# Optimization experiments

Measured on AMD Instinct MI355X. Metric: run time of the kernel, lower is better.

The kernel has to match this reference:

```python
import jax, jax.numpy as jnp
import numpy as np

N_NODES = 50000
N_EDGES = 400000
N_GRAPHS = 256
HID = 128
FEAT_IN, POS_IN, EDGE_IN = 64, 16, 16
N_LAYERS = 4


def _lin(x, w, b):
    return x @ w.T + b


def setup_inputs() -> dict:
    key = jax.random.key(0)
    ks = iter(jax.random.split(key, 64))
    s = 0.05

    def w(shape):
        return (jax.random.normal(next(ks), shape, dtype=jnp.float32) * s)

    inp = {
        "h": jax.random.normal(next(ks), (N_NODES, FEAT_IN), dtype=jnp.float32),
        "e": jax.random.normal(next(ks), (N_EDGES, EDGE_IN), dtype=jnp.float32),
        "p": jax.random.normal(next(ks), (N_NODES, POS_IN), dtype=jnp.float32),
        "edge_index": jax.random.randint(next(ks), (2, N_EDGES), 0, N_NODES),
        "batch": jnp.sort(jax.random.randint(next(ks), (N_NODES,), 0, N_GRAPHS)),
        # embeddings
        "h_embed_w": w((HID, FEAT_IN)), "h_embed_b": w((HID,)),
        "e_embed_w": w((HID, EDGE_IN)), "e_embed_b": w((HID,)),
        "p_embed_w": w((HID, POS_IN)), "p_embed_b": w((HID,)),
        # per-layer params, stacked over layers
        "hu_w": w((N_LAYERS, HID, 5 * HID)), "hu_b": w((N_LAYERS, HID)),
        "eu_w": w((N_LAYERS, HID, 3 * HID)), "eu_b": w((N_LAYERS, HID)),
        "pu_w": w((N_LAYERS, HID, 3 * HID)), "pu_b": w((N_LAYERS, HID)),
        "hagg_w": w((N_LAYERS, HID, 2 * HID)), "hagg_b": w((N_LAYERS, HID)),
        "pagg_w": w((N_LAYERS, HID, 2 * HID)), "pagg_b": w((N_LAYERS, HID)),
        # readout MLP
        "r1_w": w((HID, 2 * HID)), "r1_b": w((HID,)),
        "r2_w": w((HID // 2, HID)), "r2_b": w((HID // 2,)),
        "r3_w": w((1, HID // 2)), "r3_b": w((1,)),
    }
    return inp


def reference(h, e, p, edge_index, batch,
              h_embed_w, h_embed_b, e_embed_w, e_embed_b, p_embed_w, p_embed_b,
              hu_w, hu_b, eu_w, eu_b, pu_w, pu_b,
              hagg_w, hagg_b, pagg_w, pagg_b,
              r1_w, r1_b, r2_w, r2_b, r3_w, r3_b):
    send, rec = edge_index[0], edge_index[1]
    N = h.shape[0]

    h = _lin(h, h_embed_w, h_embed_b)
    e = _lin(e, e_embed_w, e_embed_b)
    p = _lin(p, p_embed_w, p_embed_b)

    for l in range(N_LAYERS):
        hp_send = jnp.concatenate((h[send], p[send]), axis=1)  # [E, 2H]
        hp_rec = jnp.concatenate((h[rec], p[rec]), axis=1)     # [E, 2H]
        h_msg = _lin(jnp.concatenate((hp_send, hp_rec, e), axis=1), hu_w[l], hu_b[l])
        h_msg_agg = jax.ops.segment_sum(h_msg, rec, num_segments=N)
        h = _lin(jnp.concatenate((h, h_msg_agg), axis=1), hagg_w[l], hagg_b[l])
        e = _lin(jnp.concatenate((h[send], h[rec], e), axis=1), eu_w[l], eu_b[l])
        p_msg = _lin(jnp.concatenate((p[send], p[rec], e), axis=1), pu_w[l], pu_b[l])
        p_msg_agg = jax.ops.segment_sum(p_msg, rec, num_segments=N)
        p = _lin(jnp.concatenate((p, p_msg_agg), axis=1), pagg_w[l], pagg_b[l])

    h_agg = jax.ops.segment_sum(h, batch, num_segments=N_GRAPHS)
    p_agg = jax.ops.segment_sum(p, batch, num_segments=N_GRAPHS)
    hep = jnp.concatenate((h_agg, p_agg), axis=1)
    x = jax.nn.relu(_lin(hep, r1_w, r1_b))
    x = jax.nn.relu(_lin(x, r2_w, r2_b))
    out = _lin(x, r3_w, r3_b).squeeze(-1)  # [N_GRAPHS]
    return (out, p)
```

## Files before the change

kernel.cpp:

```cpp
#include <hip/hip_runtime.h>

typedef __attribute__((ext_vector_type(8))) short bf16x8;
typedef __attribute__((ext_vector_type(4))) float f32x4;
typedef __attribute__((ext_vector_type(4))) unsigned short us4;
typedef __attribute__((ext_vector_type(2))) unsigned short us2;

__device__ __forceinline__ float b2f(unsigned short h) {
  union { unsigned int u; float f; } v; v.u = ((unsigned int)h) << 16; return v.f;
}
__device__ __forceinline__ unsigned short f2b(float f) {
  union { float f; unsigned int u; } v; v.f = f;
  unsigned int r = v.u + 0x7fffu + ((v.u >> 16) & 1u);
  return (unsigned short)(r >> 16);
}

__global__ void f2b_kernel(const float* __restrict__ in, unsigned short* __restrict__ out, int n4) {
  int i = blockIdx.x * blockDim.x + threadIdx.x;
  int stride = gridDim.x * blockDim.x;
  for (; i < n4; i += stride) {
    float4 v = reinterpret_cast<const float4*>(in)[i];
    us4 o;
    o[0] = f2b(v.x); o[1] = f2b(v.y); o[2] = f2b(v.z); o[3] = f2b(v.w);
    reinterpret_cast<us4*>(out)[i] = o;
  }
}

__launch_bounds__(256)
__global__ void compose_w(const float* __restrict__ hg, const float* __restrict__ hu,
                          const float* __restrict__ pg, const float* __restrict__ pu,
                          const float* __restrict__ hub, const float* __restrict__ pub,
                          unsigned short* __restrict__ wh, unsigned short* __restrict__ wp,
                          float* __restrict__ bh, float* __restrict__ bp) {
  __shared__ float As[128][129];
  __shared__ float Bs[128][132];
  __shared__ float bvs[128];
  const int l = blockIdx.x >> 3, t = blockIdx.x & 7;
  const float* A; const float* B; const float* bv; unsigned short* W; float* bo;
  int lda, ldb, K2, ldw, cbase;
  if (t < 5) {
    A = hg + (size_t)l * 128 * 256; lda = 256;
    B = hu + (size_t)l * 128 * 640; ldb = 640; K2 = 640;
    W = wh + (size_t)l * 128 * 768; ldw = 768;
    bv = hub + l * 128; bo = bh + l * 128; cbase = t * 128;
  } else {
    A = pg + (size_t)l * 128 * 256; lda = 256;
    B = pu + (size_t)l * 128 * 384; ldb = 384; K2 = 384;
    W = wp + (size_t)l * 128 * 512; ldw = 512;
    bv = pub + l * 128; bo = bp + l * 128; cbase = (t - 5) * 128;
  }
  const int tid = threadIdx.x;
  for (int idx = tid; idx < 128 * 128; idx += 256) {
    int r = idx >> 7, c = idx & 127;
    As[r][c] = A[r * lda + 128 + c];
    Bs[r][c] = B[r * ldb + cbase + c];
  }
  if (tid < 128) bvs[tid] = bv[tid];
  __syncthreads();
  const int o = tid & 127, g = tid >> 7;
  float acc[64];
#pragma unroll
  for (int j = 0; j < 64; ++j) acc[j] = 0.f;
  for (int m = 0; m < 128; ++m) {
    float a = As[o][m];
#pragma unroll
    for (int j4 = 0; j4 < 16; ++j4) {
      float4 b4 = *reinterpret_cast<const float4*>(&Bs[m][g * 64 + j4 * 4]);
      acc[j4 * 4 + 0] += a * b4.x; acc[j4 * 4 + 1] += a * b4.y;
      acc[j4 * 4 + 2] += a * b4.z; acc[j4 * 4 + 3] += a * b4.w;
    }
  }
#pragma unroll
  for (int j4 = 0; j4 < 16; ++j4) {
    us4 ov;
    ov[0] = f2b(acc[j4 * 4 + 0]); ov[1] = f2b(acc[j4 * 4 + 1]);
    ov[2] = f2b(acc[j4 * 4 + 2]); ov[3] = f2b(acc[j4 * 4 + 3]);
    *reinterpret_cast<us4*>(&W[(long)o * ldw + cbase + g * 64 + j4 * 4]) = ov;
  }
  if (cbase == 0) {
    for (int idx = tid; idx < 128 * 128; idx += 256) {
      int oo = idx >> 7, m = idx & 127;
      W[(long)oo * ldw + K2 + m] = f2b(A[oo * lda + m]);
    }
    if (tid < 128) {
      float s = 0.f;
      for (int m = 0; m < 128; ++m) s += As[tid][m] * bvs[m];
      bo[tid] = s;
    }
  }
}

template<int K>
__launch_bounds__(256)
__global__ void embed_fast(const float* __restrict__ in, const float* __restrict__ w,
                           const float* __restrict__ b, unsigned short* __restrict__ out,
                           long M, int ostride, int ocoloff, const float* __restrict__ degB,
                           unsigned short* __restrict__ out2, const float* __restrict__ scaleF) {
  __shared__ float wT[K][129];
  __shared__ float xt[16 * K];
  const int tid = threadIdx.x;
  const int col = tid & 127;
  const int half = tid >> 7;
  for (int idx = tid; idx < 128 * K; idx += 256) {
    int c = idx / K, k = idx % K;
    wT[k][c] = w[idx];
  }
  __syncthreads();
  float wreg[K];
#pragma unroll
  for (int k = 0; k < K; ++k) wreg[k] = wT[k][col];
  const float bcol = b[col];

  for (long r0 = (long)blockIdx.x * 16; r0 < M; r0 += (long)gridDim.x * 16) {
    __syncthreads();
    const float4* src4 = reinterpret_cast<const float4*>(in + r0 * K);
    const int n4 = 16 * K / 4;
    if (r0 + 16 <= M) {
      for (int i = tid; i < n4; i += 256)
        reinterpret_cast<float4*>(xt)[i] = src4[i];
    } else {
      int rem = (int)((M - r0) * K) / 4;
      for (int i = tid; i < n4; i += 256) {
        float4 z = {0.f, 0.f, 0.f, 0.f};
        reinterpret_cast<float4*>(xt)[i] = (i < rem) ? src4[i] : z;
      }
    }
    __syncthreads();
#pragma unroll
    for (int rr = 0; rr < 8; ++rr) {
      long row = r0 + half * 8 + rr;
      if (row >= M) break;
      const float* xr = &xt[(half * 8 + rr) * K];
      float acc = bcol * (degB ? degB[row] : 1.0f);
#pragma unroll
      for (int k4 = 0; k4 < K / 4; ++k4) {
        float4 xv = reinterpret_cast<const float4*>(xr)[k4];
        acc += xv.x * wreg[k4 * 4] + xv.y * wreg[k4 * 4 + 1] +
               xv.z * wreg[k4 * 4 + 2] + xv.w * wreg[k4 * 4 + 3];
      }
      long o = row * ostride + ocoloff + col;
      out[o] = f2b(acc);
      if (out2) out2[o] = f2b(acc * scaleF[row]);
    }
  }
}

__global__ void count_deg(const int* __restrict__ rec, int* __restrict__ deg, int E) {
  int i = blockIdx.x * blockDim.x + threadIdx.x;
  if (i < E) atomicAdd(&deg[rec[i]], 1);
}

__global__ void scan_blk(const int* __restrict__ deg, int* __restrict__ tmp,
                         int* __restrict__ blkSum, int N) {
  __shared__ int ts[256];
  const int b = blockIdx.x, t = threadIdx.x;
  const int base = b * 1024 + t * 4;
  int v0 = (base + 0 < N) ? deg[base + 0] : 0;
  int v1 = (base + 1 < N) ? deg[base + 1] : 0;
  int v2 = (base + 2 < N) ? deg[base + 2] : 0;
  int v3 = (base + 3 < N) ? deg[base + 3] : 0;
  int tsum = v0 + v1 + v2 + v3;
  ts[t] = tsum;
  __syncthreads();
  for (int off = 1; off < 256; off <<= 1) {
    int x = (t >= off) ? ts[t - off] : 0;
    __syncthreads();
    ts[t] += x;
    __syncthreads();
  }
  int texcl = ts[t] - tsum;
  if (base + 0 < N) tmp[base + 0] = texcl;
  if (base + 1 < N) tmp[base + 1] = texcl + v0;
  if (base + 2 < N) tmp[base + 2] = texcl + v0 + v1;
  if (base + 3 < N) tmp[base + 3] = texcl + v0 + v1 + v2;
  if (t == 255) blkSum[b] = ts[255];
}

__global__ void scan_top(int* __restrict__ blkSum, int nb) {
  __shared__ int s[64];
  int t = threadIdx.x;
  if (t < nb) s[t] = blkSum[t];
  __syncthreads();
  if (t == 0) {
    int run = 0;
    for (int i = 0; i < nb; ++i) { int x = s[i]; s[i] = run; run += x; }
  }
  __syncthreads();
  if (t < nb) blkSum[t] = s[t];
}

__global__ void scan_fix(const int* __restrict__ deg, int* __restrict__ row_ptr,
                         const int* __restrict__ blkOff, int* __restrict__ cursor,
                         float* __restrict__ degF, int N, int E) {
  const int b = blockIdx.x, t = threadIdx.x;
  const int base = b * 1024 + t * 4;
  const int off = blkOff[b];
#pragma unroll
  for (int k = 0; k < 4; ++k) {
    int i = base + k;
    if (i < N) {
      int v = row_ptr[i] + off;
      row_ptr[i] = v;
      cursor[i] = v;
      degF[i] = (float)deg[i];
    }
  }
  if (b == 0 && t == 0) row_ptr[N] = E;
}

__global__ void scatter_perm(const int* __restrict__ rec, const int* __restrict__ send,
                             int* __restrict__ cursor, int* __restrict__ perm,
                             int* __restrict__ sendP, int E) {
  int i = blockIdx.x * blockDim.x + threadIdx.x;
  if (i < E) {
    int pos = atomicAdd(&cursor[rec[i]], 1);
    perm[pos] = i;
    sendP[pos] = send[i];
  }
}

__global__ void segsum_raw(const float* __restrict__ eraw, const int* __restrict__ row_ptr,
                           const int* __restrict__ perm, float* __restrict__ out16, int N) {
  int sub = threadIdx.x >> 4;
  int f = threadIdx.x & 15;
  int r = blockIdx.x * 16 + sub;
  if (r >= N) return;
  int j0 = row_ptr[r], j1 = row_ptr[r + 1];
  float s0 = 0.f, s1 = 0.f;
  int j = j0;
  for (; j + 2 <= j1; j += 2) {
    int e0 = perm[j], e1 = perm[j + 1];
    s0 += eraw[(long)e0 * 16 + f];
    s1 += eraw[(long)e1 * 16 + f];
  }
  if (j < j1) s0 += eraw[(long)perm[j] * 16 + f];
  out16[(long)r * 16 + f] = s0 + s1;
}

__launch_bounds__(256)
__global__ void gather_sum256(const unsigned short* __restrict__ src,
                              const int* __restrict__ row_ptr, const int* __restrict__ sendP,
                              unsigned short* __restrict__ dst, int N) {
  const int wid = threadIdx.x >> 6, lane = threadIdx.x & 63;
  const int r = blockIdx.x * 4 + wid;
  if (r >= N) return;
  const int j0 = row_ptr[r], j1 = row_ptr[r + 1];
  const int off = lane * 4;
  float a0 = 0.f, a1 = 0.f, a2 = 0.f, a3 = 0.f;
  int j = j0;
  for (; j + 2 <= j1; j += 2) {
    int i0 = sendP[j], i1 = sendP[j + 1];
    us4 x = *reinterpret_cast<const us4*>(&src[(long)i0 * 256 + off]);
    us4 y = *reinterpret_cast<const us4*>(&src[(long)i1 * 256 + off]);
    a0 += b2f(x[0]) + b2f(y[0]); a1 += b2f(x[1]) + b2f(y[1]);
    a2 += b2f(x[2]) + b2f(y[2]); a3 += b2f(x[3]) + b2f(y[3]);
  }
  if (j < j1) {
    us4 x = *reinterpret_cast<const us4*>(&src[(long)sendP[j] * 256 + off]);
    a0 += b2f(x[0]); a1 += b2f(x[1]); a2 += b2f(x[2]); a3 += b2f(x[3]);
  }
  us4 o;
  o[0] = f2b(a0); o[1] = f2b(a1); o[2] = f2b(a2); o[3] = f2b(a3);
  *reinterpret_cast<us4*>(&dst[(long)r * 256 + off]) = o;
}

__launch_bounds__(256)
__global__ void gather_sum128(const unsigned short* __restrict__ src, int col,
                              const int* __restrict__ row_ptr, const int* __restrict__ sendP,
                              unsigned short* __restrict__ dst, int N) {
  const int wid = threadIdx.x >> 6, lane = threadIdx.x & 63;
  const int r = blockIdx.x * 4 + wid;
  if (r >= N) return;
  const int j0 = row_ptr[r], j1 = row_ptr[r + 1];
  const int half = lane >> 5;
  const int c = lane & 31;
  const int off = col + c * 4;
  float a0 = 0.f, a1 = 0.f, a2 = 0.f, a3 = 0.f;
  float b0 = 0.f, b1 = 0.f, b2 = 0.f, b3 = 0.f;
  int j = j0 + half;
  for (; j + 2 < j1; j += 4) {
    int i0 = sendP[j], i1 = sendP[j + 2];
    us4 x = *reinterpret_cast<const us4*>(&src[(long)i0 * 256 + off]);
    us4 y = *reinterpret_cast<const us4*>(&src[(long)i1 * 256 + off]);
    a0 += b2f(x[0]); a1 += b2f(x[1]); a2 += b2f(x[2]); a3 += b2f(x[3]);
    b0 += b2f(y[0]); b1 += b2f(y[1]); b2 += b2f(y[2]); b3 += b2f(y[3]);
  }
  if (j < j1) {
    us4 x = *reinterpret_cast<const us4*>(&src[(long)sendP[j] * 256 + off]);
    a0 += b2f(x[0]); a1 += b2f(x[1]); a2 += b2f(x[2]); a3 += b2f(x[3]);
  }
  a0 += b0; a1 += b1; a2 += b2; a3 += b3;
  a0 += __shfl_xor(a0, 32); a1 += __shfl_xor(a1, 32);
  a2 += __shfl_xor(a2, 32); a3 += __shfl_xor(a3, 32);
  if (half == 0) {
    us4 o;
    o[0] = f2b(a0); o[1] = f2b(a1); o[2] = f2b(a2); o[3] = f2b(a3);
    *reinterpret_cast<us4*>(&dst[(long)r * 256 + off]) = o;
  }
}

__launch_bounds__(256, 3)
__global__ void gemm_mp(int M, int nsrc, int strides, int coloffs,
                        const unsigned short* __restrict__ sp0, const unsigned short* __restrict__ sp1,
                        const unsigned short* __restrict__ sp2, const unsigned short* __restrict__ sp3,
                        const unsigned short* __restrict__ sp4, const unsigned short* __restrict__ sp5,
                        const unsigned short* __restrict__ Wb,
                        const float* __restrict__ bdeg, const float* __restrict__ bone,
                        const float* __restrict__ degF,
                        unsigned short* __restrict__ outB, int ostride, int ocoloff,
                        unsigned short* __restrict__ outB2, float* __restrict__ outF) {
  __shared__ __align__(16) unsigned short ldsW[8 * 64 * 8];
  const int tid = threadIdx.x;
  const int wid = tid >> 6, lane = tid & 63;
  const int K = nsrc * 128;
  const long rowBase = (long)blockIdx.x * 128 + wid * 32;
  const int lq = lane >> 4;
  const int lr = lane & 15;

  int rowD[2];
#pragma unroll
  for (int am = 0; am < 2; ++am) {
    long e = rowBase + am * 16 + lr;
    if (e >= M) e = M - 1;
    rowD[am] = (int)e;
  }

  f32x4 acc[2][8];
#pragma unroll
  for (int i = 0; i < 2; ++i)
#pragma unroll
    for (int j = 0; j < 8; ++j) acc[i][j] = 0.f;

  for (int si = 0; si < nsrc; ++si) {
    const unsigned short* sp = (si == 0) ? sp0 : (si == 1) ? sp1 : (si == 2) ? sp2
                              : (si == 3) ? sp3 : (si == 4) ? sp4 : sp5;
    const long astride = (long)(((strides >> (si * 4)) & 15) * 128);
    const int acoloff = ((coloffs >> (si * 4)) & 15) * 128;
#pragma unroll
    for (int sub = 0; sub < 4; ++sub) {
      const int koff = acoloff + sub * 32 + lq * 8;
      bf16x8 a[2];
#pragma unroll
      for (int am = 0; am < 2; ++am)
        a[am] = *reinterpret_cast<const bf16x8*>(&sp[(long)rowD[am] * astride + koff]);
      __syncthreads();
#pragma unroll
      for (int it = 0; it < 2; ++it) {
        int idx = tid + it * 256;
        int t = idx >> 6, l = idx & 63;
        int n = t * 16 + (l & 15);
        int kk = si * 128 + sub * 32 + ((l >> 4) * 8);
        *reinterpret_cast<bf16x8*>(&ldsW[idx * 8]) =
            *reinterpret_cast<const bf16x8*>(&Wb[(long)n * K + kk]);
      }
      __syncthreads();
#pragma unroll
      for (int n = 0; n < 8; ++n) {
        bf16x8 b = *reinterpret_cast<const bf16x8*>(&ldsW[(n * 64 + lane) * 8]);
#pragma unroll
        for (int am = 0; am < 2; ++am)
          acc[am][n] = __builtin_amdgcn_mfma_f32_16x16x32_bf16(a[am], b, acc[am][n], 0, 0, 0);
      }
    }
  }

  float bd[8], bo[8];
#pragma unroll
  for (int n = 0; n < 8; ++n) {
    bd[n] = bdeg ? bdeg[n * 16 + lr] : 0.f;
    bo[n] = bone ? bone[n * 16 + lr] : 0.f;
  }

#pragma unroll
  for (int am = 0; am < 2; ++am) {
#pragma unroll
    for (int r = 0; r < 4; ++r) {
      long row = rowBase + am * 16 + lq * 4 + r;
      if (row < M) {
        float d = degF[row];
        long ob = row * ostride + ocoloff;
#pragma unroll
        for (int n = 0; n < 8; ++n) {
          float v = acc[am][n][r] + bd[n] * d + bo[n];
          outB[ob + n * 16 + lr] = f2b(v);
          if (outB2) outB2[ob + n * 16 + lr] = f2b(v * d);
          if (outF) outF[row * 128 + n * 16 + lr] = v;
        }
      }
    }
  }
}

__global__ void readout_agg(const unsigned short* __restrict__ hp,
                            const int* __restrict__ batch, float* __restrict__ hep, int N) {
  int col = threadIdx.x;
  int n0 = blockIdx.x * 128;
  int n1 = n0 + 128; if (n1 > N) n1 = N;
  float sum = 0.f; int curg = -1;
  for (int n = n0; n < n1; ++n) {
    int g = batch[n];
    if (g != curg) {
      if (curg >= 0) unsafeAtomicAdd(&hep[(long)curg * 256 + col], sum);
      curg = g; sum = 0.f;
    }
    sum += b2f(hp[(long)n * 256 + col]);
  }
  if (curg >= 0) unsafeAtomicAdd(&hep[(long)curg * 256 + col], sum);
}

__global__ void mlp_kernel(const float* __restrict__ hep,
                           const float* __restrict__ r1w, const float* __restrict__ r1b,
                           const float* __restrict__ r2w, const float* __restrict__ r2b,
                           const float* __restrict__ r3w, const float* __restrict__ r3b,
                           float* __restrict__ out) {
  int g = blockIdx.x, t = threadIdx.x;
  __shared__ float x[256];
  __shared__ float y[128];
  __shared__ float z[64];
  x[t] = hep[(long)g * 256 + t];
  x[t + 128] = hep[(long)g * 256 + 128 + t];
  __syncthreads();
  float s = r1b[t];
  for (int k = 0; k < 256; ++k) s += r1w[t * 256 + k] * x[k];
  y[t] = fmaxf(s, 0.f);
  __syncthreads();
  if (t < 64) {
    float s2 = r2b[t];
    for (int k = 0; k < 128; ++k) s2 += r2w[t * 128 + k] * y[k];
    z[t] = fmaxf(s2, 0.f);
  }
  __syncthreads();
  if (t == 0) {
    float s3 = r3b[0];
    for (int k = 0; k < 64; ++k) s3 += r3w[k] * z[k];
    out[g] = s3;
  }
}

extern "C" void kernel_launch(void* const* d_in, const int* in_sizes, int n_in,
                              void* d_out, int out_size, void* d_ws, size_t ws_size,
                              hipStream_t stream) {
  const float* h_in = (const float*)d_in[0];
  const float* e_in = (const float*)d_in[1];
  const float* p_in = (const float*)d_in[2];
  const int* ei = (const int*)d_in[3];
  const int* batch = (const int*)d_in[4];
  const float* he_w = (const float*)d_in[5];  const float* he_b = (const float*)d_in[6];
  const float* ee_w = (const float*)d_in[7];  const float* ee_b = (const float*)d_in[8];
  const float* pe_w = (const float*)d_in[9];  const float* pe_b = (const float*)d_in[10];
  const float* hu_w = (const float*)d_in[11]; const float* hu_b = (const float*)d_in[12];
  const float* eu_w = (const float*)d_in[13]; const float* eu_b = (const float*)d_in[14];
  const float* pu_w = (const float*)d_in[15]; const float* pu_b = (const float*)d_in[16];
  const float* hg_w = (const float*)d_in[17]; const float* hg_b = (const float*)d_in[18];
  const float* pg_w = (const float*)d_in[19]; const float* pg_b = (const float*)d_in[20];
  const float* r1w = (const float*)d_in[21];  const float* r1b = (const float*)d_in[22];
  const float* r2w = (const float*)d_in[23];  const float* r2b = (const float*)d_in[24];
  const float* r3w = (const float*)d_in[25];  const float* r3b = (const float*)d_in[26];

  const int N = 50000, E = 400000, G = 256;
  const int* send = ei;
  const int* rec = ei + E;

  char* ws = (char*)d_ws;
  size_t off = 0;
  auto alloc = [&](size_t bytes) {
    void* pp = ws + off;
    off += (bytes + 255) & ~(size_t)255;
    return pp;
  };
  unsigned short* hp  = (unsigned short*)alloc((size_t)N * 256 * 2);
  unsigned short* dhp = (unsigned short*)alloc((size_t)N * 256 * 2);
  unsigned short* gHP = (unsigned short*)alloc((size_t)N * 256 * 2);
  unsigned short* sT  = (unsigned short*)alloc((size_t)N * 128 * 2);
  float* segsumF = (float*)alloc((size_t)N * 16 * 4);
  int* deg = (int*)alloc((size_t)N * 4);
  int* row_ptr = (int*)alloc((size_t)(N + 1) * 4);
  int* cursor = (int*)alloc((size_t)N * 4);
  int* blkSum = (int*)alloc((size_t)64 * 4);
  int* perm = (int*)alloc((size_t)E * 4);
  int* sendP = (int*)alloc((size_t)E * 4);
  float* degF = (float*)alloc((size_t)N * 4);
  float* hep = (float*)alloc((size_t)G * 256 * 4);
  unsigned short* w_h2 = (unsigned short*)alloc((size_t)4 * 128 * 768 * 2);
  unsigned short* w_p2 = (unsigned short*)alloc((size_t)4 * 128 * 512 * 2);
  unsigned short* w_eu = (unsigned short*)alloc((size_t)4 * 128 * 384 * 2);
  float* bh1 = (float*)alloc((size_t)4 * 128 * 4);
  float* bp1 = (float*)alloc((size_t)4 * 128 * 4);
  (void)ws_size; (void)n_in; (void)in_sizes; (void)out_size;

  f2b_kernel<<<192, 256, 0, stream>>>(eu_w, w_eu, 4 * 128 * 384 / 4);
  compose_w<<<32, 256, 0, stream>>>(hg_w, hu_w, pg_w, pu_w, hu_b, pu_b, w_h2, w_p2, bh1, bp1);

  const int nb = (N + 1023) / 1024;
  hipMemsetAsync(deg, 0, (size_t)N * 4, stream);
  count_deg<<<(E + 255) / 256, 256, 0, stream>>>(rec, deg, E);
  scan_blk<<<nb, 256, 0, stream>>>(deg, row_ptr, blkSum, N);
  scan_top<<<1, 64, 0, stream>>>(blkSum, nb);
  scan_fix<<<nb, 256, 0, stream>>>(deg, row_ptr, blkSum, cursor, degF, N, E);
  scatter_perm<<<(E + 255) / 256, 256, 0, stream>>>(rec, send, cursor, perm, sendP, E);

  embed_fast<64><<<3125, 256, 0, stream>>>(h_in, he_w, he_b, hp, N, 256, 0, nullptr, dhp, degF);
  embed_fast<16><<<3125, 256, 0, stream>>>(p_in, pe_w, pe_b, hp, N, 256, 128, nullptr, dhp, degF);
  segsum_raw<<<(N + 15) / 16, 256, 0, stream>>>(e_in, row_ptr, perm, segsumF, N);
  embed_fast<16><<<3125, 256, 0, stream>>>(segsumF, ee_w, ee_b, sT, N, 128, 0, degF, nullptr, nullptr);

  gather_sum256<<<(N + 3) / 4, 256, 0, stream>>>(hp, row_ptr, sendP, gHP, N);

  float* pOut = (float*)d_out + 256;
  const int gridN = (N + 127) / 128;
  const int gridG = (N + 3) / 4;

  for (int l = 0; l < 4; ++l) {
    gemm_mp<<<gridN, 256, 0, stream>>>(N, 6, 0x212222, 0x001010,
        gHP, gHP, dhp, dhp, sT, hp,
        w_h2 + (size_t)l * 128 * 768, bh1 + l * 128, hg_b + l * 128, degF,
        hp, 256, 0, dhp, nullptr);
    gather_sum128<<<gridG, 256, 0, stream>>>(hp, 0, row_ptr, sendP, gHP, N);
    gemm_mp<<<gridN, 256, 0, stream>>>(N, 3, 0x122, 0x000,
        gHP, dhp, sT, nullptr, nullptr, nullptr,
        w_eu + (size_t)l * 128 * 384, eu_b + l * 128, nullptr, degF,
        sT, 128, 0, nullptr, nullptr);
    gemm_mp<<<gridN, 256, 0, stream>>>(N, 4, 0x2122, 0x1011,
        gHP, dhp, sT, hp, nullptr, nullptr,
        w_p2 + (size_t)l * 128 * 512, bp1 + l * 128, pg_b + l * 128, degF,
        hp, 256, 128, (l < 3) ? dhp : nullptr, (l == 3) ? pOut : nullptr);
    if (l < 3)
      gather_sum128<<<gridG, 256, 0, stream>>>(hp, 128, row_ptr, sendP, gHP, N);
  }

  hipMemsetAsync(hep, 0, (size_t)G * 256 * 4, stream);
  readout_agg<<<(N + 127) / 128, 256, 0, stream>>>(hp, batch, hep, N);
  mlp_kernel<<<G, 128, 0, stream>>>(hep, r1w, r1b, r2w, r2b, r3w, r3b, (float*)d_out);
}
```

Measured before the change: 724.6 us.

## Drop degree-scaled copy buffer; apply degree scaling via separate MFMA accumulator

Removes the dhp buffer, which held degree-scaled copies of node features and was written by the embed and GEMM epilogues. Sources that need scaling now go into a second accumulator set (accS), and the epilogue multiplies that by degree before adding it. This cuts one bf16 store stream per GEMM and per embed, at the cost of double the accumulator registers, which may reduce occupancy under launch_bounds(256,3). It also splits compose_w into 128 smaller blocks for more parallelism, and scaling in fp32 rather than bf16 slightly changes rounding.

```diff
diff --git a/kernel.cpp b/kernel.cpp
--- a/kernel.cpp
+++ b/kernel.cpp
@@ -3,7 +3,6 @@
 typedef __attribute__((ext_vector_type(8))) short bf16x8;
 typedef __attribute__((ext_vector_type(4))) float f32x4;
 typedef __attribute__((ext_vector_type(4))) unsigned short us4;
-typedef __attribute__((ext_vector_type(2))) unsigned short us2;
 
 __device__ __forceinline__ float b2f(unsigned short h) {
   union { unsigned int u; float f; } v; v.u = ((unsigned int)h) << 16; return v.f;
@@ -32,49 +31,52 @@
                           unsigned short* __restrict__ wh, unsigned short* __restrict__ wp,
                           float* __restrict__ bh, float* __restrict__ bp) {
   __shared__ float As[128][129];
-  __shared__ float Bs[128][132];
+  __shared__ float Bs[128][36];
   __shared__ float bvs[128];
-  const int l = blockIdx.x >> 3, t = blockIdx.x & 7;
+  const int l = blockIdx.x >> 5, t = blockIdx.x & 31;
   const float* A; const float* B; const float* bv; unsigned short* W; float* bo;
   int lda, ldb, K2, ldw, cbase;
-  if (t < 5) {
+  if (t < 20) {
     A = hg + (size_t)l * 128 * 256; lda = 256;
     B = hu + (size_t)l * 128 * 640; ldb = 640; K2 = 640;
     W = wh + (size_t)l * 128 * 768; ldw = 768;
-    bv = hub + l * 128; bo = bh + l * 128; cbase = t * 128;
+    bv = hub + l * 128; bo = bh + l * 128; cbase = t * 32;
   } else {
     A = pg + (size_t)l * 128 * 256; lda = 256;
     B = pu + (size_t)l * 128 * 384; ldb = 384; K2 = 384;
     W = wp + (size_t)l * 128 * 512; ldw = 512;
-    bv = pub + l * 128; bo = bp + l * 128; cbase = (t - 5) * 128;
+    bv = pub + l * 128; bo = bp + l * 128; cbase = (t - 20) * 32;
   }
   const int tid = threadIdx.x;
   for (int idx = tid; idx < 128 * 128; idx += 256) {
     int r = idx >> 7, c = idx & 127;
     As[r][c] = A[r * lda + 128 + c];
-    Bs[r][c] = B[r * ldb + cbase + c];
+  }
+  for (int idx = tid; idx < 128 * 32; idx += 256) {
+    int m = idx >> 5, c = idx & 31;
+    Bs[m][c] = B[m * ldb + cbase + c];
   }
   if (tid < 128) bvs[tid] = bv[tid];
   __syncthreads();
   const int o = tid & 127, g = tid >> 7;
-  float acc[64];
-#pragma unroll
-  for (int j = 0; j < 64; ++j) acc[j] = 0.f;
+  float acc[16];
+#pragma unroll
+  for (int j = 0; j < 16; ++j) acc[j] = 0.f;
   for (int m = 0; m < 128; ++m) {
     float a = As[o][m];
 #pragma unroll
-    for (int j4 = 0; j4 < 16; ++j4) {
-      float4 b4 = *reinterpret_cast<const float4*>(&Bs[m][g * 64 + j4 * 4]);
+    for (int j4 = 0; j4 < 4; ++j4) {
+      float4 b4 = *reinterpret_cast<const float4*>(&Bs[m][g * 16 + j4 * 4]);
       acc[j4 * 4 + 0] += a * b4.x; acc[j4 * 4 + 1] += a * b4.y;
       acc[j4 * 4 + 2] += a * b4.z; acc[j4 * 4 + 3] += a * b4.w;
     }
   }
 #pragma unroll
-  for (int j4 = 0; j4 < 16; ++j4) {
+  for (int j4 = 0; j4 < 4; ++j4) {
     us4 ov;
     ov[0] = f2b(acc[j4 * 4 + 0]); ov[1] = f2b(acc[j4 * 4 + 1]);
     ov[2] = f2b(acc[j4 * 4 + 2]); ov[3] = f2b(acc[j4 * 4 + 3]);
-    *reinterpret_cast<us4*>(&W[(long)o * ldw + cbase + g * 64 + j4 * 4]) = ov;
+    *reinterpret_cast<us4*>(&W[(long)o * ldw + cbase + g * 16 + j4 * 4]) = ov;
   }
   if (cbase == 0) {
     for (int idx = tid; idx < 128 * 128; idx += 256) {
@@ -93,8 +95,7 @@
 __launch_bounds__(256)
 __global__ void embed_fast(const float* __restrict__ in, const float* __restrict__ w,
                            const float* __restrict__ b, unsigned short* __restrict__ out,
-                           long M, int ostride, int ocoloff, const float* __restrict__ degB,
-                           unsigned short* __restrict__ out2, const float* __restrict__ scaleF) {
+                           long M, int ostride, int ocoloff, const float* __restrict__ degB) {
   __shared__ float wT[K][129];
   __shared__ float xt[16 * K];
   const int tid = threadIdx.x;
@@ -137,9 +138,7 @@
         acc += xv.x * wreg[k4 * 4] + xv.y * wreg[k4 * 4 + 1] +
                xv.z * wreg[k4 * 4 + 2] + xv.w * wreg[k4 * 4 + 3];
       }
-      long o = row * ostride + ocoloff + col;
-      out[o] = f2b(acc);
-      if (out2) out2[o] = f2b(acc * scaleF[row]);
+      out[row * ostride + ocoloff + col] = f2b(acc);
     }
   }
 }
@@ -299,7 +298,7 @@
 }
 
 __launch_bounds__(256, 3)
-__global__ void gemm_mp(int M, int nsrc, int strides, int coloffs,
+__global__ void gemm_mp(int M, int nsrc, int strides, int coloffs, int smask,
                         const unsigned short* __restrict__ sp0, const unsigned short* __restrict__ sp1,
                         const unsigned short* __restrict__ sp2, const unsigned short* __restrict__ sp3,
                         const unsigned short* __restrict__ sp4, const unsigned short* __restrict__ sp5,
@@ -307,7 +306,7 @@
                         const float* __restrict__ bdeg, const float* __restrict__ bone,
                         const float* __restrict__ degF,
                         unsigned short* __restrict__ outB, int ostride, int ocoloff,
-                        unsigned short* __restrict__ outB2, float* __restrict__ outF) {
+                        float* __restrict__ outF) {
   __shared__ __align__(16) unsigned short ldsW[8 * 64 * 8];
   const int tid = threadIdx.x;
   const int wid = tid >> 6, lane = tid & 63;
@@ -324,17 +323,18 @@
     rowD[am] = (int)e;
   }
 
-  f32x4 acc[2][8];
+  f32x4 acc[2][8], accS[2][8];
 #pragma unroll
   for (int i = 0; i < 2; ++i)
 #pragma unroll
-    for (int j = 0; j < 8; ++j) acc[i][j] = 0.f;
+    for (int j = 0; j < 8; ++j) { acc[i][j] = 0.f; accS[i][j] = 0.f; }
 
   for (int si = 0; si < nsrc; ++si) {
     const unsigned short* sp = (si == 0) ? sp0 : (si == 1) ? sp1 : (si == 2) ? sp2
                               : (si == 3) ? sp3 : (si == 4) ? sp4 : sp5;
     const long astride = (long)(((strides >> (si * 4)) & 15) * 128);
     const int acoloff = ((coloffs >> (si * 4)) & 15) * 128;
+    const bool sc = (smask >> si) & 1;
 #pragma unroll
     for (int sub = 0; sub < 4; ++sub) {
       const int koff = acoloff + sub * 32 + lq * 8;
@@ -353,12 +353,22 @@
             *reinterpret_cast<const bf16x8*>(&Wb[(long)n * K + kk]);
       }
       __syncthreads();
-#pragma unroll
-      for (int n = 0; n < 8; ++n) {
-        bf16x8 b = *reinterpret_cast<const bf16x8*>(&ldsW[(n * 64 + lane) * 8]);
-#pragma unroll
-        for (int am = 0; am < 2; ++am)
-          acc[am][n] = __builtin_amdgcn_mfma_f32_16x16x32_bf16(a[am], b, acc[am][n], 0, 0, 0);
+      if (sc) {
+#pragma unroll
+        for (int n = 0; n < 8; ++n) {
+          bf16x8 b = *reinterpret_cast<const bf16x8*>(&ldsW[(n * 64 + lane) * 8]);
+#pragma unroll
+          for (int am = 0; am < 2; ++am)
+            accS[am][n] = __builtin_amdgcn_mfma_f32_16x16x32_bf16(a[am], b, accS[am][n], 0, 0, 0);
+        }
+      } else {
+#pragma unroll
+        for (int n = 0; n < 8; ++n) {
+          bf16x8 b = *reinterpret_cast<const bf16x8*>(&ldsW[(n * 64 + lane) * 8]);
+#pragma unroll
+          for (int am = 0; am < 2; ++am)
+            acc[am][n] = __builtin_amdgcn_mfma_f32_16x16x32_bf16(a[am], b, acc[am][n], 0, 0, 0);
+        }
       }
     }
   }
@@ -380,9 +390,8 @@
         long ob = row * ostride + ocoloff;
 #pragma unroll
         for (int n = 0; n < 8; ++n) {
-          float v = acc[am][n][r] + bd[n] * d + bo[n];
+          float v = acc[am][n][r] + d * accS[am][n][r] + bd[n] * d + bo[n];
           outB[ob + n * 16 + lr] = f2b(v);
-          if (outB2) outB2[ob + n * 16 + lr] = f2b(v * d);
           if (outF) outF[row * 128 + n * 16 + lr] = v;
         }
       }
@@ -468,7 +477,6 @@
     return pp;
   };
   unsigned short* hp  = (unsigned short*)alloc((size_t)N * 256 * 2);
-  unsigned short* dhp = (unsigned short*)alloc((size_t)N * 256 * 2);
   unsigned short* gHP = (unsigned short*)alloc((size_t)N * 256 * 2);
   unsigned short* sT  = (unsigned short*)alloc((size_t)N * 128 * 2);
   float* segsumF = (float*)alloc((size_t)N * 16 * 4);
@@ -488,7 +496,7 @@
   (void)ws_size; (void)n_in; (void)in_sizes; (void)out_size;
 
   f2b_kernel<<<192, 256, 0, stream>>>(eu_w, w_eu, 4 * 128 * 384 / 4);
-  compose_w<<<32, 256, 0, stream>>>(hg_w, hu_w, pg_w, pu_w, hu_b, pu_b, w_h2, w_p2, bh1, bp1);
+  compose_w<<<128, 256, 0, stream>>>(hg_w, hu_w, pg_w, pu_w, hu_b, pu_b, w_h2, w_p2, bh1, bp1);
 
   const int nb = (N + 1023) / 1024;
   hipMemsetAsync(deg, 0, (size_t)N * 4, stream);
@@ -498,10 +506,10 @@
   scan_fix<<<nb, 256, 0, stream>>>(deg, row_ptr, blkSum, cursor, degF, N, E);
   scatter_perm<<<(E + 255) / 256, 256, 0, stream>>>(rec, send, cursor, perm, sendP, E);
 
-  embed_fast<64><<<3125, 256, 0, stream>>>(h_in, he_w, he_b, hp, N, 256, 0, nullptr, dhp, degF);
-  embed_fast<16><<<3125, 256, 0, stream>>>(p_in, pe_w, pe_b, hp, N, 256, 128, nullptr, dhp, degF);
+  embed_fast<64><<<3125, 256, 0, stream>>>(h_in, he_w, he_b, hp, N, 256, 0, nullptr);
+  embed_fast<16><<<3125, 256, 0, stream>>>(p_in, pe_w, pe_b, hp, N, 256, 128, nullptr);
   segsum_raw<<<(N + 15) / 16, 256, 0, stream>>>(e_in, row_ptr, perm, segsumF, N);
-  embed_fast<16><<<3125, 256, 0, stream>>>(segsumF, ee_w, ee_b, sT, N, 128, 0, degF, nullptr, nullptr);
+  embed_fast<16><<<3125, 256, 0, stream>>>(segsumF, ee_w, ee_b, sT, N, 128, 0, degF);
 
   gather_sum256<<<(N + 3) / 4, 256, 0, stream>>>(hp, row_ptr, sendP, gHP, N);
 
@@ -510,19 +518,19 @@
   const int gridG = (N + 3) / 4;
 
   for (int l = 0; l < 4; ++l) {
-    gemm_mp<<<gridN, 256, 0, stream>>>(N, 6, 0x212222, 0x001010,
-        gHP, gHP, dhp, dhp, sT, hp,
+    gemm_mp<<<gridN, 256, 0, stream>>>(N, 6, 0x212222, 0x001010, 0x0C,
+        gHP, gHP, hp, hp, sT, hp,
         w_h2 + (size_t)l * 128 * 768, bh1 + l * 128, hg_b + l * 128, degF,
-        hp, 256, 0, dhp, nullptr);
+        hp, 256, 0, nullptr);
     gather_sum128<<<gridG, 256, 0, stream>>>(hp, 0, row_ptr, sendP, gHP, N);
-    gemm_mp<<<gridN, 256, 0, stream>>>(N, 3, 0x122, 0x000,
-        gHP, dhp, sT, nullptr, nullptr, nullptr,
+    gemm_mp<<<gridN, 256, 0, stream>>>(N, 3, 0x122, 0x000, 0x2,
+        gHP, hp, sT, nullptr, nullptr, nullptr,
         w_eu + (size_t)l * 128 * 384, eu_b + l * 128, nullptr, degF,
-        sT, 128, 0, nullptr, nullptr);
-    gemm_mp<<<gridN, 256, 0, stream>>>(N, 4, 0x2122, 0x1011,
-        gHP, dhp, sT, hp, nullptr, nullptr,
+        sT, 128, 0, nullptr);
+    gemm_mp<<<gridN, 256, 0, stream>>>(N, 4, 0x2122, 0x1011, 0x2,
+        gHP, hp, sT, hp, nullptr, nullptr,
         w_p2 + (size_t)l * 128 * 512, bp1 + l * 128, pg_b + l * 128, degF,
-        hp, 256, 128, (l < 3) ? dhp : nullptr, (l == 3) ? pOut : nullptr);
+        hp, 256, 128, (l == 3) ? pOut : nullptr);
     if (l < 3)
       gather_sum128<<<gridG, 256, 0, stream>>>(hp, 128, row_ptr, sendP, gHP, N);
   }
```

New measurement: 1.384 ms. 91.1% more time.
